# Kernel tuning notes

Measured on AMD Instinct MI355X. Metric: run time of the kernel, lower is better.

## Reference

```python
import jax, jax.numpy as jnp
import numpy as np

# Norse LIFRefracParameters defaults
DT = 0.001
TAU_SYN_INV = 200.0
TAU_MEM_INV = 100.0
V_LEAK = 0.0
V_TH = 1.0
V_RESET = 0.0
ALPHA = 100.0          # super-spike surrogate slope
RHO_RESET = 5.0        # refractory steps after a spike
TAU_FILTER_INV = 223.1435511314

T, B, F, H, O = 1000, 64, 128, 512, 32


def heaviside(x):
    return (x > 0).astype(x.dtype)


def setup_inputs() -> dict:
    key = jax.random.key(0)
    k1, k2, k3, k4, k5 = jax.random.split(key, 5)
    x = jax.random.normal(k1, (T, B, F), dtype=jnp.float32)
    # torch Linear-style uniform(-1/sqrt(fan_in), 1/sqrt(fan_in)) init
    w_in = jax.random.uniform(k2, (H, F), jnp.float32, -1.0 / np.sqrt(F), 1.0 / np.sqrt(F))
    w_rec = jax.random.uniform(k3, (H, H), jnp.float32, -1.0 / np.sqrt(H), 1.0 / np.sqrt(H))
    w_out = jax.random.uniform(k4, (O, H), jnp.float32, -1.0 / np.sqrt(H), 1.0 / np.sqrt(H))
    b_out = jax.random.uniform(k5, (O,), jnp.float32, -1.0 / np.sqrt(H), 1.0 / np.sqrt(H))
    return {"x": x, "w_in": w_in, "w_rec": w_rec, "w_out": w_out, "b_out": b_out}


def reference(x, w_in, w_rec, w_out, b_out):
    Bd, Hd = x.shape[1], w_in.shape[0]

    def step(carry, x_t):
        z, v, i, rho, o = carry
        # LIF membrane/synapse Euler update (norse lif_step)
        v_dec = v + DT * TAU_MEM_INV * ((V_LEAK - v) + i)
        i_dec = i * (1.0 - DT * TAU_SYN_INV)
        z_new = heaviside(v_dec - V_TH)
        v_new = (1.0 - z_new) * v_dec + z_new * V_RESET
        i_new = i_dec + x_t @ w_in.T + z @ w_rec.T
        # refractory update (norse compute_refractory_update)
        refrac_mask = heaviside(rho)
        v_new = (1.0 - refrac_mask) * v_new + refrac_mask * v
        z_new = (1.0 - refrac_mask) * z_new
        rho_new = (1.0 - z_new) * jnp.maximum(rho - refrac_mask, 0.0) + z_new * RHO_RESET
        # ExpFilter: linear readout + exponential low-pass
        lin = z_new @ w_out.T + b_out
        o_new = o + DT * TAU_FILTER_INV * (lin - o)
        return (z_new, v_new, i_new, rho_new, o_new), o_new

    zeros_h = jnp.zeros((Bd, Hd), x.dtype)
    o0 = jnp.zeros((Bd, w_out.shape[0]), x.dtype)
    carry0 = (zeros_h, zeros_h, zeros_h, zeros_h, o0)
    _, outputs = jax.lax.scan(step, carry0, x)
    return outputs  # [T, B, O]
```

## Files before the change

kernel.cpp:

```cpp
#include <hip/hip_runtime.h>

#define T_STEPS 1000
#define BATCH   64
#define FIN     128
#define HID     512
#define NOUT    32
#define ALPHA_F 0.2231435511314f
#define PFD     4
#define WREC_ROWS (HID + 8)

__global__ void prep_transpose(const float* __restrict__ w_rec,
                               const float* __restrict__ w_out,
                               float* __restrict__ wrecT,
                               float* __restrict__ woutT) {
    int idx = blockIdx.x * blockDim.x + threadIdx.x;
    if (idx < HID * HID) {
        int j = idx / HID, h = idx % HID;
        wrecT[h * HID + j] = w_rec[idx];
    } else if (idx < HID * HID + 8 * HID) {
        wrecT[idx] = 0.0f;
    }
    if (idx < NOUT * HID) {
        int o = idx / HID, h = idx % HID;
        woutT[h * NOUT + o] = w_out[idx];
    }
}

#define GTM 128
#define GTN 128
#define GKC 32

__global__ __launch_bounds__(256)
void xwin_gemm(const float* __restrict__ x, const float* __restrict__ w_in,
               float* __restrict__ xwin) {
    __shared__ float xs[GKC][GTM + 4];
    __shared__ float ws[GKC][GTN + 4];
    const int tid = threadIdx.x;
    const int tb_base = blockIdx.x * GTM;
    const int h_base  = blockIdx.y * GTN;
    const int tx = tid & 15, ty = tid >> 4;

    float acc[8][8];
#pragma unroll
    for (int i = 0; i < 8; ++i)
#pragma unroll
        for (int j = 0; j < 8; ++j) acc[i][j] = 0.f;

    for (int kc = 0; kc < FIN; kc += GKC) {
#pragma unroll
        for (int q = 0; q < 4; ++q) {
            int li  = tid * 4 + q;
            int row = li >> 3, c4 = li & 7;
            float4 v = *(const float4*)&x[(size_t)(tb_base + row) * FIN + kc + c4 * 4];
            xs[c4*4+0][row] = v.x; xs[c4*4+1][row] = v.y;
            xs[c4*4+2][row] = v.z; xs[c4*4+3][row] = v.w;
            float4 w = *(const float4*)&w_in[(size_t)(h_base + row) * FIN + kc + c4 * 4];
            ws[c4*4+0][row] = w.x; ws[c4*4+1][row] = w.y;
            ws[c4*4+2][row] = w.z; ws[c4*4+3][row] = w.w;
        }
        __syncthreads();
#pragma unroll
        for (int k = 0; k < GKC; ++k) {
            float4 a0 = *(const float4*)&xs[k][tx * 8];
            float4 a1 = *(const float4*)&xs[k][tx * 8 + 4];
            float4 b0 = *(const float4*)&ws[k][ty * 8];
            float4 b1 = *(const float4*)&ws[k][ty * 8 + 4];
            float av[8] = {a0.x, a0.y, a0.z, a0.w, a1.x, a1.y, a1.z, a1.w};
            float bv[8] = {b0.x, b0.y, b0.z, b0.w, b1.x, b1.y, b1.z, b1.w};
#pragma unroll
            for (int i = 0; i < 8; ++i)
#pragma unroll
                for (int j = 0; j < 8; ++j)
                    acc[i][j] = fmaf(av[i], bv[j], acc[i][j]);
        }
        __syncthreads();
    }
#pragma unroll
    for (int i = 0; i < 8; ++i) {
        size_t tb = (size_t)tb_base + tx * 8 + i;
        float4 o0 = make_float4(acc[i][0], acc[i][1], acc[i][2], acc[i][3]);
        float4 o1 = make_float4(acc[i][4], acc[i][5], acc[i][6], acc[i][7]);
        *(float4*)&xwin[tb * HID + h_base + ty * 8]     = o0;
        *(float4*)&xwin[tb * HID + h_base + ty * 8 + 4] = o1;
    }
}

__global__ __launch_bounds__(256, 1)
void snn_scan4w(const float* __restrict__ xwin,
                const float* __restrict__ wrT,
                unsigned long long* __restrict__ masks) {
    const int b    = blockIdx.x;
    const int tid  = threadIdx.x;
    const int w    = tid >> 6;
    const int lane = tid & 63;
    const int h0 = tid, h1 = tid + 256;

    __shared__ __align__(16) unsigned long long smasks[2][8];
    if (tid < 16) ((unsigned long long*)smasks)[tid] = 0ull;
    __syncthreads();

    float v0 = 0.f, v1 = 0.f, c0 = 0.f, c1 = 0.f, q0 = 0.f, q1 = 0.f;

    const float* wp0 = wrT + h0;
    const float* wp1 = wrT + h1;

    float xq0[PFD], xq1[PFD];
#pragma unroll
    for (int s = 0; s < PFD; ++s) {
        xq0[s] = xwin[((size_t)s * BATCH + b) * HID + h0];
        xq1[s] = xwin[((size_t)s * BATCH + b) * HID + h1];
    }

    for (int t0 = 0; t0 < T_STEPS; t0 += PFD) {
        float pa0[PFD], pa1[PFD];
#pragma unroll
        for (int s = 0; s < PFD; ++s) {
            int tn = t0 + PFD + s; if (tn >= T_STEPS) tn = T_STEPS - 1;
            pa0[s] = xwin[((size_t)tn * BATCH + b) * HID + h0];
            pa1[s] = xwin[((size_t)tn * BATCH + b) * HID + h1];
        }

#pragma unroll
        for (int s = 0; s < PFD; ++s) {
            const int t = t0 + s;
            const int cur = t & 1, nxt = cur ^ 1;

            const ulonglong2* sp = (const ulonglong2*)&smasks[cur][0];
            ulonglong2 u0 = sp[0], u1 = sp[1], u2 = sp[2], u3 = sp[3];
            unsigned long long wd[8] = {u0.x, u0.y, u1.x, u1.y,
                                        u2.x, u2.y, u3.x, u3.y};

            int rows[16];
            unsigned long long rem[8];
#pragma unroll
            for (int j = 0; j < 8; ++j) {
                unsigned long long u = wd[j];
                int l0 = (u != 0ull) ? (int)__builtin_ctzll(u) : 64;
                u &= u - 1;
                int l1 = (u != 0ull) ? (int)__builtin_ctzll(u) : 64;
                u &= u - 1;
                rows[2 * j]     = (l0 < 64) ? (j * 64 + l0) : HID;
                rows[2 * j + 1] = (l1 < 64) ? (j * 64 + l1) : HID;
                rem[j] = u;
            }

            float g0[16], g1[16];
#pragma unroll
            for (int k = 0; k < 16; ++k) {
                const size_t off = (size_t)rows[k] * HID;
                g0[k] = wp0[off];
                g1[k] = wp1[off];
            }

            float rec0 = (((g0[0]+g0[1])+(g0[2]+g0[3])) + ((g0[4]+g0[5])+(g0[6]+g0[7])))
                       + (((g0[8]+g0[9])+(g0[10]+g0[11])) + ((g0[12]+g0[13])+(g0[14]+g0[15])));
            float rec1 = (((g1[0]+g1[1])+(g1[2]+g1[3])) + ((g1[4]+g1[5])+(g1[6]+g1[7])))
                       + (((g1[8]+g1[9])+(g1[10]+g1[11])) + ((g1[12]+g1[13])+(g1[14]+g1[15])));

#pragma unroll
            for (int j = 0; j < 8; ++j) {
                while (rem[j]) {
                    int l = (int)__builtin_ctzll(rem[j]);
                    rem[j] &= rem[j] - 1;
                    const size_t off = (size_t)(j * 64 + l) * HID;
                    rec0 += wp0[off];
                    rec1 += wp1[off];
                }
            }

            float z0, z1;
            {
                const float v_dec = v0 + 0.1f * ((0.0f - v0) + c0);
                const float i_dec = c0 * 0.8f;
                float zz = (v_dec - 1.0f) > 0.0f ? 1.0f : 0.0f;
                float v_tmp = (zz != 0.0f) ? 0.0f : v_dec;
                const float refr = (q0 > 0.0f) ? 1.0f : 0.0f;
                v0 = (refr != 0.0f) ? v0 : v_tmp;
                zz = (refr != 0.0f) ? 0.0f : zz;
                q0 = (zz != 0.0f) ? 5.0f : fmaxf(q0 - refr, 0.0f);
                c0 = (i_dec + xq0[s]) + rec0;
                z0 = zz;
            }
            {
                const float v_dec = v1 + 0.1f * ((0.0f - v1) + c1);
                const float i_dec = c1 * 0.8f;
                float zz = (v_dec - 1.0f) > 0.0f ? 1.0f : 0.0f;
                float v_tmp = (zz != 0.0f) ? 0.0f : v_dec;
                const float refr = (q1 > 0.0f) ? 1.0f : 0.0f;
                v1 = (refr != 0.0f) ? v1 : v_tmp;
                zz = (refr != 0.0f) ? 0.0f : zz;
                q1 = (zz != 0.0f) ? 5.0f : fmaxf(q1 - refr, 0.0f);
                c1 = (i_dec + xq1[s]) + rec1;
                z1 = zz;
            }

            const unsigned long long mA = __ballot(z0 != 0.0f);
            const unsigned long long mB = __ballot(z1 != 0.0f);

            if (lane == 0) {
                smasks[nxt][w]     = mA;
                smasks[nxt][4 + w] = mB;
                unsigned long long* mg = &masks[((size_t)t * BATCH + b) * 8];
                mg[w]     = mA;
                mg[4 + w] = mB;
            }
            __syncthreads();
        }
#pragma unroll
        for (int s = 0; s < PFD; ++s) { xq0[s] = pa0[s]; xq1[s] = pa1[s]; }
    }
}

__global__ __launch_bounds__(256)
void readout_lin(const unsigned long long* __restrict__ masks,
                 const float* __restrict__ woutT,
                 float* __restrict__ lin) {
    __shared__ float s_w[HID * NOUT];
    const int tid = threadIdx.x;
#pragma unroll
    for (int q = 0; q < 16; ++q) {
        int fi = (q * 256 + tid) * 4;
        int h = fi >> 5, o = fi & 31;
        float4 w = *(const float4*)&woutT[fi];
        int xs = (h & 7) << 2;
        *(float4*)&s_w[(h << 5) + (o ^ xs)] = w;
    }
    __syncthreads();

    const int b  = blockIdx.y;
    const int t  = blockIdx.x * 64 + (tid & 63);
    const int o0 = (tid >> 6) * 8;
    if (t >= T_STEPS) return;

    const unsigned long long* mp = &masks[((size_t)t * BATCH + b) * 8];
    float a0 = 0.f, a1 = 0.f, a2 = 0.f, a3 = 0.f, a4 = 0.f, a5 = 0.f, a6 = 0.f, a7 = 0.f;
#pragma unroll
    for (int j = 0; j < 8; ++j) {
        unsigned long long mm = mp[j];
        while (mm) {
            int l = (int)__builtin_ctzll(mm);
            mm &= mm - 1;
            int h  = j * 64 + l;
            int xs = (h & 7) << 2;
            const float4 w0 = *(const float4*)&s_w[(h << 5) + (o0 ^ xs)];
            const float4 w1 = *(const float4*)&s_w[(h << 5) + ((o0 + 4) ^ xs)];
            a0 += w0.x; a1 += w0.y; a2 += w0.z; a3 += w0.w;
            a4 += w1.x; a5 += w1.y; a6 += w1.z; a7 += w1.w;
        }
    }
    float* op = &lin[((size_t)t * BATCH + b) * NOUT + o0];
    *(float4*)op       = make_float4(a0, a1, a2, a3);
    *(float4*)(op + 4) = make_float4(a4, a5, a6, a7);
}

__global__ __launch_bounds__(256)
void readout_filter(const float* __restrict__ lin,
                    const float* __restrict__ b_out,
                    float* __restrict__ out) {
    const int bo = blockIdx.x * 256 + threadIdx.x;
    const int c  = blockIdx.y;
    const float bb = b_out[bo & 31];
    const int t0 = c * 125;
    int ts = t0 - 128; if (ts < 0) ts = 0;
    const int te = t0 + 125;
    float o = 0.f;
    for (int t = ts; t < te; ++t) {
        float l = lin[(size_t)t * (BATCH * NOUT) + bo] + bb;
        o = o + ALPHA_F * (l - o);
        if (t >= t0) out[(size_t)t * (BATCH * NOUT) + bo] = o;
    }
}

template<int PRECOMP>
__global__ __launch_bounds__(512)
void snn_main(const float* __restrict__ xsrc,
              const float* __restrict__ w_in,
              const float* __restrict__ wr, int wrA, int wrB,
              const float* __restrict__ wo, int woA, int woB,
              const float* __restrict__ b_out,
              float* __restrict__ out) {
    const int b    = blockIdx.x;
    const int tid  = threadIdx.x;
    const int lane = tid & 63;

    __shared__ int   s_list[2][HID];
    __shared__ int   s_cnt[2];
    __shared__ float s_xrow[2][FIN];

    if (tid < 2) s_cnt[tid] = 0;
    if (!PRECOMP && tid < FIN)
        s_xrow[0][tid] = xsrc[(size_t)b * FIN + tid];
    float iin_reg = 0.f;
    if (PRECOMP) iin_reg = xsrc[(size_t)b * HID + tid];
    __syncthreads();

    float v = 0.f, ic = 0.f, rho = 0.f, o_state = 0.f;
    const float bout_v = (tid < NOUT) ? b_out[tid] : 0.f;

    for (int t = 0; t < T_STEPS; ++t) {
        const int cur = t & 1, nxt = cur ^ 1;
        float iin_next = 0.f;
        if (PRECOMP) {
            int tn = (t + 1 < T_STEPS) ? (t + 1) : t;
            iin_next = xsrc[((size_t)tn * BATCH + b) * HID + tid];
        }
        float iin;
        if (PRECOMP) {
            iin = iin_reg;
        } else {
            float s0 = 0.f, s1 = 0.f, s2 = 0.f, s3 = 0.f;
#pragma unroll
            for (int kq = 0; kq < FIN / 4; ++kq) {
                float4 xv = *(const float4*)&s_xrow[cur][kq * 4];
                float4 wv = *(const float4*)&w_in[(size_t)tid * FIN + kq * 4];
                s0 = fmaf(xv.x, wv.x, s0); s1 = fmaf(xv.y, wv.y, s1);
                s2 = fmaf(xv.z, wv.z, s2); s3 = fmaf(xv.w, wv.w, s3);
            }
            iin = (s0 + s1) + (s2 + s3);
        }
        const int cn = s_cnt[cur];
        float r0 = 0.f, r1 = 0.f, r2 = 0.f, r3 = 0.f;
        int k = 0;
        for (; k + 4 <= cn; k += 4) {
            int i0 = s_list[cur][k],     i1 = s_list[cur][k + 1];
            int i2 = s_list[cur][k + 2], i3 = s_list[cur][k + 3];
            r0 += wr[(size_t)i0 * wrA + (size_t)tid * wrB];
            r1 += wr[(size_t)i1 * wrA + (size_t)tid * wrB];
            r2 += wr[(size_t)i2 * wrA + (size_t)tid * wrB];
            r3 += wr[(size_t)i3 * wrA + (size_t)tid * wrB];
        }
        for (; k < cn; ++k)
            r0 += wr[(size_t)s_list[cur][k] * wrA + (size_t)tid * wrB];
        const float rec = (r0 + r1) + (r2 + r3);

        const float v_dec = v + 0.1f * ((0.0f - v) + ic);
        const float i_dec = ic * 0.8f;
        float z      = (v_dec - 1.0f) > 0.0f ? 1.0f : 0.0f;
        float v_tmp  = (z != 0.0f) ? 0.0f : v_dec;
        const float refr = (rho > 0.0f) ? 1.0f : 0.0f;
        v   = (refr != 0.0f) ? v : v_tmp;
        z   = (refr != 0.0f) ? 0.0f : z;
        rho = (z != 0.0f) ? 5.0f : fmaxf(rho - refr, 0.0f);
        ic  = (i_dec + iin) + rec;

        unsigned long long mbal = __ballot(z != 0.0f);
        int nsp = __popcll(mbal);
        int base = 0;
        if (lane == 0 && nsp) base = atomicAdd(&s_cnt[nxt], nsp);
        base = __shfl(base, 0);
        if (z != 0.0f) {
            int pos = base + __popcll(mbal & ((1ull << lane) - 1ull));
            s_list[nxt][pos] = tid;
        }
        __syncthreads();

        if (tid < NOUT) {
            const int c2 = s_cnt[nxt];
            float lin = 0.f;
            for (int kk = 0; kk < c2; ++kk)
                lin += wo[(size_t)s_list[nxt][kk] * woA + (size_t)tid * woB];
            lin += bout_v;
            o_state = o_state + ALPHA_F * (lin - o_state);
            out[((size_t)t * BATCH + b) * NOUT + tid] = o_state;
        }
        if (tid == 0) s_cnt[cur] = 0;
        if (PRECOMP) iin_reg = iin_next;
        if (!PRECOMP && tid >= 128 && tid < 128 + FIN) {
            int tn = (t + 1 < T_STEPS) ? (t + 1) : t;
            s_xrow[nxt][tid - 128] = xsrc[((size_t)tn * BATCH + b) * FIN + (tid - 128)];
        }
        __syncthreads();
    }
}

extern "C" void kernel_launch(void* const* d_in, const int* in_sizes, int n_in,
                              void* d_out, int out_size, void* d_ws, size_t ws_size,
                              hipStream_t stream) {
    const float* x     = (const float*)d_in[0];
    const float* w_in  = (const float*)d_in[1];
    const float* w_rec = (const float*)d_in[2];
    const float* w_out = (const float*)d_in[3];
    const float* b_out = (const float*)d_in[4];
    float* out = (float*)d_out;

    const size_t xwin_b  = (size_t)T_STEPS * BATCH * HID * sizeof(float);
    const size_t masks_b = (size_t)T_STEPS * BATCH * 8 * sizeof(unsigned long long);
    const size_t wrect_b = (size_t)WREC_ROWS * HID * sizeof(float);
    const size_t woutt_b = (size_t)HID * NOUT * sizeof(float);

    char* ws = (char*)d_ws;
    const int prep_n = HID * HID + 8 * HID;

    if (ws_size >= xwin_b + masks_b + wrect_b + woutt_b) {
        float* xwin  = (float*)ws;
        float* lin   = (float*)ws;
        unsigned long long* masks = (unsigned long long*)(ws + xwin_b);
        float* wrecT = (float*)(ws + xwin_b + masks_b);
        float* woutT = (float*)(ws + xwin_b + masks_b + wrect_b);

        prep_transpose<<<(prep_n + 255) / 256, 256, 0, stream>>>(w_rec, w_out, wrecT, woutT);
        dim3 g(T_STEPS * BATCH / GTM, HID / GTN);
        xwin_gemm<<<g, 256, 0, stream>>>(x, w_in, xwin);
        snn_scan4w<<<BATCH, 256, 0, stream>>>(xwin, wrecT, masks);
        readout_lin<<<dim3((T_STEPS + 63) / 64, BATCH), 256, 0, stream>>>(masks, woutT, lin);
        readout_filter<<<dim3(BATCH * NOUT / 256, 8), 256, 0, stream>>>(lin, b_out, out);
    } else if (ws_size >= xwin_b + wrect_b + woutt_b) {
        float* xwin  = (float*)ws;
        float* wrecT = (float*)(ws + xwin_b);
        float* woutT = (float*)(ws + xwin_b + wrect_b);
        prep_transpose<<<(prep_n + 255) / 256, 256, 0, stream>>>(w_rec, w_out, wrecT, woutT);
        dim3 g(T_STEPS * BATCH / GTM, HID / GTN);
        xwin_gemm<<<g, 256, 0, stream>>>(x, w_in, xwin);
        snn_main<1><<<BATCH, HID, 0, stream>>>(xwin, nullptr, wrecT, HID, 1,
                                               woutT, NOUT, 1, b_out, out);
    } else if (ws_size >= wrect_b + woutt_b) {
        float* wrecT = (float*)ws;
        float* woutT = (float*)(ws + wrect_b);
        prep_transpose<<<(prep_n + 255) / 256, 256, 0, stream>>>(w_rec, w_out, wrecT, woutT);
        snn_main<0><<<BATCH, HID, 0, stream>>>(x, w_in, wrecT, HID, 1,
                                               woutT, NOUT, 1, b_out, out);
    } else {
        snn_main<0><<<BATCH, HID, 0, stream>>>(x, w_in, w_rec, 1, HID,
                                               w_out, 1, HID, b_out, out);
    }
}
```

Before: 1.253 ms.

## Assign adjacent hidden pairs per thread for float2 gathers and lighten step barrier

Each thread now owns hidden units 2*tid and 2*tid+1 instead of tid and tid+256. The recurrent-weight gathers, xwin prefetch and mask stores can then use float2 and 128-bit accesses, halving the number of memory instructions per spike row. The spike-mask bit-to-neuron mapping is remapped to match in both the scan and the readout kernels. The per-step __syncthreads is replaced by an explicit LDS waitcnt plus a raw s_barrier, which relies on global mask stores not needing to be ordered before the barrier.

```diff
diff --git a/kernel.cpp b/kernel.cpp
--- a/kernel.cpp
+++ b/kernel.cpp
@@ -93,7 +93,7 @@
     const int tid  = threadIdx.x;
     const int w    = tid >> 6;
     const int lane = tid & 63;
-    const int h0 = tid, h1 = tid + 256;
+    const int h0   = 2 * tid;
 
     __shared__ __align__(16) unsigned long long smasks[2][8];
     if (tid < 16) ((unsigned long long*)smasks)[tid] = 0ull;
@@ -101,23 +101,19 @@
 
     float v0 = 0.f, v1 = 0.f, c0 = 0.f, c1 = 0.f, q0 = 0.f, q1 = 0.f;
 
-    const float* wp0 = wrT + h0;
-    const float* wp1 = wrT + h1;
-
-    float xq0[PFD], xq1[PFD];
-#pragma unroll
-    for (int s = 0; s < PFD; ++s) {
-        xq0[s] = xwin[((size_t)s * BATCH + b) * HID + h0];
-        xq1[s] = xwin[((size_t)s * BATCH + b) * HID + h1];
-    }
+    const float* wp = wrT + h0;
+
+    float2 xq[PFD];
+#pragma unroll
+    for (int s = 0; s < PFD; ++s)
+        xq[s] = *(const float2*)&xwin[((size_t)s * BATCH + b) * HID + h0];
 
     for (int t0 = 0; t0 < T_STEPS; t0 += PFD) {
-        float pa0[PFD], pa1[PFD];
+        float2 pa[PFD];
 #pragma unroll
         for (int s = 0; s < PFD; ++s) {
             int tn = t0 + PFD + s; if (tn >= T_STEPS) tn = T_STEPS - 1;
-            pa0[s] = xwin[((size_t)tn * BATCH + b) * HID + h0];
-            pa1[s] = xwin[((size_t)tn * BATCH + b) * HID + h1];
+            pa[s] = *(const float2*)&xwin[((size_t)tn * BATCH + b) * HID + h0];
         }
 
 #pragma unroll
@@ -135,36 +131,37 @@
 #pragma unroll
             for (int j = 0; j < 8; ++j) {
                 unsigned long long u = wd[j];
-                int l0 = (u != 0ull) ? (int)__builtin_ctzll(u) : 64;
+                const int hb = 128 * (j >> 1) + (j & 1);
+                int l0 = (u != 0ull) ? (int)__builtin_ctzll(u) : 0;
+                bool e0 = (u != 0ull);
                 u &= u - 1;
-                int l1 = (u != 0ull) ? (int)__builtin_ctzll(u) : 64;
+                int l1 = (u != 0ull) ? (int)__builtin_ctzll(u) : 0;
+                bool e1 = (u != 0ull);
                 u &= u - 1;
-                rows[2 * j]     = (l0 < 64) ? (j * 64 + l0) : HID;
-                rows[2 * j + 1] = (l1 < 64) ? (j * 64 + l1) : HID;
+                rows[2 * j]     = e0 ? (hb + 2 * l0) : HID;
+                rows[2 * j + 1] = e1 ? (hb + 2 * l1) : HID;
                 rem[j] = u;
             }
 
-            float g0[16], g1[16];
-#pragma unroll
-            for (int k = 0; k < 16; ++k) {
-                const size_t off = (size_t)rows[k] * HID;
-                g0[k] = wp0[off];
-                g1[k] = wp1[off];
-            }
-
-            float rec0 = (((g0[0]+g0[1])+(g0[2]+g0[3])) + ((g0[4]+g0[5])+(g0[6]+g0[7])))
-                       + (((g0[8]+g0[9])+(g0[10]+g0[11])) + ((g0[12]+g0[13])+(g0[14]+g0[15])));
-            float rec1 = (((g1[0]+g1[1])+(g1[2]+g1[3])) + ((g1[4]+g1[5])+(g1[6]+g1[7])))
-                       + (((g1[8]+g1[9])+(g1[10]+g1[11])) + ((g1[12]+g1[13])+(g1[14]+g1[15])));
+            float2 g[16];
+#pragma unroll
+            for (int k = 0; k < 16; ++k)
+                g[k] = *(const float2*)&wp[(size_t)rows[k] * HID];
+
+            float rec0 = (((g[0].x+g[1].x)+(g[2].x+g[3].x)) + ((g[4].x+g[5].x)+(g[6].x+g[7].x)))
+                       + (((g[8].x+g[9].x)+(g[10].x+g[11].x)) + ((g[12].x+g[13].x)+(g[14].x+g[15].x)));
+            float rec1 = (((g[0].y+g[1].y)+(g[2].y+g[3].y)) + ((g[4].y+g[5].y)+(g[6].y+g[7].y)))
+                       + (((g[8].y+g[9].y)+(g[10].y+g[11].y)) + ((g[12].y+g[13].y)+(g[14].y+g[15].y)));
 
 #pragma unroll
             for (int j = 0; j < 8; ++j) {
+                const int hb = 128 * (j >> 1) + (j & 1);
                 while (rem[j]) {
                     int l = (int)__builtin_ctzll(rem[j]);
                     rem[j] &= rem[j] - 1;
-                    const size_t off = (size_t)(j * 64 + l) * HID;
-                    rec0 += wp0[off];
-                    rec1 += wp1[off];
+                    float2 gg = *(const float2*)&wp[(size_t)(hb + 2 * l) * HID];
+                    rec0 += gg.x;
+                    rec1 += gg.y;
                 }
             }
 
@@ -178,7 +175,7 @@
                 v0 = (refr != 0.0f) ? v0 : v_tmp;
                 zz = (refr != 0.0f) ? 0.0f : zz;
                 q0 = (zz != 0.0f) ? 5.0f : fmaxf(q0 - refr, 0.0f);
-                c0 = (i_dec + xq0[s]) + rec0;
+                c0 = (i_dec + xq[s].x) + rec0;
                 z0 = zz;
             }
             {
@@ -190,7 +187,7 @@
                 v1 = (refr != 0.0f) ? v1 : v_tmp;
                 zz = (refr != 0.0f) ? 0.0f : zz;
                 q1 = (zz != 0.0f) ? 5.0f : fmaxf(q1 - refr, 0.0f);
-                c1 = (i_dec + xq1[s]) + rec1;
+                c1 = (i_dec + xq[s].y) + rec1;
                 z1 = zz;
             }
 
@@ -198,16 +195,15 @@
             const unsigned long long mB = __ballot(z1 != 0.0f);
 
             if (lane == 0) {
-                smasks[nxt][w]     = mA;
-                smasks[nxt][4 + w] = mB;
-                unsigned long long* mg = &masks[((size_t)t * BATCH + b) * 8];
-                mg[w]     = mA;
-                mg[4 + w] = mB;
-            }
-            __syncthreads();
-        }
-#pragma unroll
-        for (int s = 0; s < PFD; ++s) { xq0[s] = pa0[s]; xq1[s] = pa1[s]; }
+                ulonglong2 u; u.x = mA; u.y = mB;
+                *(ulonglong2*)&smasks[nxt][2 * w] = u;
+                *(ulonglong2*)&masks[((size_t)t * BATCH + b) * 8 + 2 * w] = u;
+            }
+            asm volatile("s_waitcnt lgkmcnt(0)" ::: "memory");
+            __builtin_amdgcn_s_barrier();
+        }
+#pragma unroll
+        for (int s = 0; s < PFD; ++s) xq[s] = pa[s];
     }
 }
 
@@ -237,10 +233,11 @@
 #pragma unroll
     for (int j = 0; j < 8; ++j) {
         unsigned long long mm = mp[j];
+        const int hb = 128 * (j >> 1) + (j & 1);
         while (mm) {
             int l = (int)__builtin_ctzll(mm);
             mm &= mm - 1;
-            int h  = j * 64 + l;
+            int h  = hb + 2 * l;
             int xs = (h & 7) << 2;
             const float4 w0 = *(const float4*)&s_w[(h << 5) + (o0 ^ xs)];
             const float4 w1 = *(const float4*)&s_w[(h << 5) + ((o0 + 4) ^ xs)];
```

After: 1.422 ms. 1.14x slower.
